# Kernel tuning notes

Measured on AMD Instinct MI355X. Metric: run time of the kernel, lower is better.

The kernel has to match this reference:

```python
import jax, jax.numpy as jnp
import numpy as np

B, L, D, T = 2, 2048, 1536, 2
INITRANGE = 0.1

def setup_inputs() -> dict:
    key = jax.random.key(0)
    k1, k2 = jax.random.split(key)
    hidden_states = jax.random.normal(k1, (B, L, D), dtype=jnp.float32)
    # decoder: Linear(2*D, T) with uniform(-0.1, 0.1) weight, zero bias
    W = jax.random.uniform(k2, (T, 2 * D), dtype=jnp.float32, minval=-INITRANGE, maxval=INITRANGE)
    b = jnp.zeros((T,), dtype=jnp.float32)
    return {"hidden_states": hidden_states, "W": W, "b": b}

def reference(hidden_states, W, b):
    # Faithful fused version of:
    #   prod = h[:,:,None,:] * h[:,None,:,:]; diff = h[:,:,None,:] - h[:,None,:,:]
    #   logits = cat(prod, diff, -1) @ W.T + b
    # Split W into the product half and the difference half.
    d = hidden_states.shape[-1]
    Wp, Wd = W[:, :d], W[:, d:]                      # [T, D] each
    # prod term: sum_d h[b,i,d] * h[b,j,d] * Wp[t,d]
    hw = jnp.einsum('bid,td->btid', hidden_states, Wp)          # [B,T,L,D]
    prod_logits = jnp.einsum('btid,bjd->bijt', hw, hidden_states)  # [B,L,L,T]
    # diff term: (h[b,i]-h[b,j]) @ Wd.T = (h@Wd.T)[b,i] - (h@Wd.T)[b,j]
    hd = jnp.einsum('bid,td->bit', hidden_states, Wd)           # [B,L,T]
    diff_logits = hd[:, :, None, :] - hd[:, None, :, :]         # [B,L,L,T]
    logits = prod_logits + diff_logits + b
    # symmetrize over the (i, j) pair axes
    logits = (logits + jnp.transpose(logits, (0, 2, 1, 3))) * 0.5
    return logits
```

## Files before the change

kernel.cpp:

```cpp
#include <hip/hip_runtime.h>
#include <hip/hip_bf16.h>
#include <stdint.h>

#define B_ 2
#define L_ 2048
#define D_ 1536
#define NT (D_ / 64)

typedef __attribute__((ext_vector_type(4))) float  f32x4;
typedef __attribute__((ext_vector_type(8))) __bf16 bf16x8;

__device__ __forceinline__ unsigned short f2bf(float f) {
  unsigned int u = __float_as_uint(f);
  u += 0x7fffu + ((u >> 16) & 1u);
  return (unsigned short)(u >> 16);
}

__global__ __launch_bounds__(256) void conv_kernel(
    const float* __restrict__ hs, const float* __restrict__ W,
    unsigned short* __restrict__ X, unsigned short* __restrict__ P) {
  const int idx  = blockIdx.x * 256 + threadIdx.x;
  const int base = idx * 4;
  const int d    = base % D_;
  const float4 h  = *(const float4*)(hs + base);
  const float4 w0 = *(const float4*)(W + d);
  const float4 w1 = *(const float4*)(W + 2 * D_ + d);
  ushort4 x, p0, p1;
  x.x  = f2bf(h.x);        x.y  = f2bf(h.y);        x.z  = f2bf(h.z);        x.w  = f2bf(h.w);
  p0.x = f2bf(h.x * w0.x); p0.y = f2bf(h.y * w0.y); p0.z = f2bf(h.z * w0.z); p0.w = f2bf(h.w * w0.w);
  p1.x = f2bf(h.x * w1.x); p1.y = f2bf(h.y * w1.y); p1.z = f2bf(h.z * w1.z); p1.w = f2bf(h.w * w1.w);
  *(ushort4*)(X + base) = x;
  *(ushort4*)(P + base) = p0;
  *(ushort4*)(P + (size_t)B_ * L_ * D_ + base) = p1;
}

__device__ __forceinline__ void gload16(const unsigned short* g, unsigned short* l) {
  __builtin_amdgcn_global_load_lds(
      (const __attribute__((address_space(1))) unsigned int*)g,
      (__attribute__((address_space(3))) unsigned int*)l, 16, 0, 0);
}

#define A0OFF 0
#define A1OFF 8192
#define B0OFF 16384
#define B1OFF 24576

__global__ __launch_bounds__(512, 2) void gemm_kernel(
    const unsigned short* __restrict__ X, const unsigned short* __restrict__ P,
    const float* __restrict__ bias, float2* __restrict__ out) {
  __shared__ unsigned short lds[65536];

  const int tid = threadIdx.x;

  const int id  = blockIdx.x;
  const int swz = (id & 7) * 32 + (id >> 3);
  const int bz  = swz >> 7;
  const int t2  = swz & 127;
  const int I0  = (t2 >> 3) * 128;
  const int J0  = (t2 & 7) * 256;

  const size_t planeB = (size_t)B_ * L_ * D_;
  const unsigned short* gA0 = P + (size_t)(bz * L_ + I0) * D_;
  const unsigned short* gA1 = gA0 + planeB;
  const unsigned short* gB0 = X + (size_t)(bz * L_ + J0) * D_;
  const unsigned short* gB1 = gB0 + (size_t)128 * D_;

  const int    sr    = tid >> 3;
  const int    sc    = (tid & 7) ^ (sr & 7);
  const size_t lgoff = (size_t)sr * D_ + (size_t)(sc * 8);
  const int    wuni  = (tid >> 6) * 512;

  const int lane = tid & 63;
  const int w    = tid >> 6;
  const int wr   = w & 1;
  const int wc   = w >> 1;
  const int lr   = lane & 15;
  const int q    = lane >> 4;
  const int swd  = lr & 7;
  const int csw0 = ((0 + q) ^ swd) * 8;
  const int csw1 = ((4 + q) ^ swd) * 8;
  int aRow[4], bRow[2];
#pragma unroll
  for (int m = 0; m < 4; ++m) aRow[m] = (wr * 64 + m * 16 + lr) * 64;
#pragma unroll
  for (int n = 0; n < 2; ++n) bRow[n] = (wc * 32 + n * 16 + lr) * 64;

  f32x4  acc[8][4] = {};
  bf16x8 aF[4][2], bF[2][2];

#define STG(REG, GBASE, KTN)                                                  \
  do {                                                                        \
    const unsigned short* g0 = (GBASE) + lgoff + (size_t)((KTN) * 64);        \
    gload16(g0,                 lds + (REG) + wuni);                          \
    gload16(g0 + (size_t)64 * D_, lds + (REG) + 4096 + wuni);                 \
  } while (0)

#define RDA(CB, MH)                                                           \
  do {                                                                        \
    _Pragma("unroll") for (int m = 0; m < 4; ++m) {                           \
      aF[m][0] = *(const bf16x8*)(lds + (CB) + (MH) * 8192 + aRow[m] + csw0); \
      aF[m][1] = *(const bf16x8*)(lds + (CB) + (MH) * 8192 + aRow[m] + csw1); \
    }                                                                         \
  } while (0)

#define RDB(CB, NH)                                                           \
  do {                                                                        \
    _Pragma("unroll") for (int n = 0; n < 2; ++n) {                           \
      bF[n][0] = *(const bf16x8*)(lds + (CB) + 16384 + (NH) * 8192 + bRow[n] + csw0); \
      bF[n][1] = *(const bf16x8*)(lds + (CB) + 16384 + (NH) * 8192 + bRow[n] + csw1); \
    }                                                                         \
  } while (0)

#define MM(MH, NH)                                                            \
  do {                                                                        \
    _Pragma("unroll") for (int kk = 0; kk < 2; ++kk)                          \
    _Pragma("unroll") for (int m = 0; m < 4; ++m)                             \
    _Pragma("unroll") for (int n = 0; n < 2; ++n)                             \
      acc[(MH) * 4 + m][(NH) * 2 + n] = __builtin_amdgcn_mfma_f32_16x16x32_bf16( \
          aF[m][kk], bF[n][kk], acc[(MH) * 4 + m][(NH) * 2 + n], 0, 0, 0);    \
  } while (0)

#define BAR()   __builtin_amdgcn_s_barrier()
#define LGKM0() asm volatile("s_waitcnt lgkmcnt(0)" ::: "memory")
#define WVM(n)  asm volatile("s_waitcnt vmcnt(" #n ")" ::: "memory")
#define PRIO1() __builtin_amdgcn_s_setprio(1)
#define PRIO0() __builtin_amdgcn_s_setprio(0)

#define KSTEP(CB, NB, KTN)                                                    \
  do {                                                                        \
                                                                      \
    RDA(CB, 0); RDB(CB, 0);                                                   \
    STG((NB) + A0OFF, gA0, KTN); STG((NB) + B0OFF, gB0, KTN);                 \
    BAR(); LGKM0();                                                           \
    PRIO1(); MM(0, 0); PRIO0();                                               \
    WVM(6); BAR();                                                            \
                                                                      \
    RDB(CB, 1);                                                               \
    STG((NB) + B1OFF, gB1, KTN);                                              \
    BAR(); LGKM0();                                                           \
    PRIO1(); MM(0, 1); PRIO0();                                               \
    WVM(6); BAR();                                                            \
                                                                      \
    RDA(CB, 1);                                                               \
    STG((NB) + A1OFF, gA1, KTN);                                              \
    BAR(); LGKM0();                                                           \
    PRIO1(); MM(1, 1); PRIO0();                                               \
    BAR();                                                                    \
                                        \
    RDB(CB, 0);                                                               \
    BAR(); LGKM0();                                                           \
    PRIO1(); MM(1, 0); PRIO0();                                               \
    WVM(4); BAR();                                                            \
  } while (0)

#define KTAIL(CB)                                                             \
  do {                                                                        \
    RDA(CB, 0); RDB(CB, 0);                                                   \
    BAR(); LGKM0();                                                           \
    PRIO1(); MM(0, 0); PRIO0();                                               \
    WVM(2); BAR();                                                            \
    RDB(CB, 1);                                                               \
    BAR(); LGKM0();                                                           \
    PRIO1(); MM(0, 1); PRIO0();                                               \
    WVM(0); BAR();                                                            \
    RDA(CB, 1);                                                               \
    BAR(); LGKM0();                                                           \
    PRIO1(); MM(1, 1); PRIO0();                                               \
    BAR();                                                                    \
    RDB(CB, 0);                                                               \
    LGKM0();                                                                  \
    PRIO1(); MM(1, 0); PRIO0();                                               \
  } while (0)

  STG(A0OFF, gA0, 0); STG(B0OFF, gB0, 0);
  STG(B1OFF, gB1, 0);
  STG(A1OFF, gA1, 0);
  WVM(4); BAR();

#pragma unroll 1
  for (int it = 0; it < 11; ++it) {
    const int kt0 = 2 * it;
    KSTEP(0,     32768, kt0 + 1);
    KSTEP(32768, 0,     kt0 + 2);
  }
  KSTEP(0, 32768, 23);
  KTAIL(32768);

#undef KSTEP
#undef KTAIL
#undef STG
#undef RDA
#undef RDB
#undef MM

  const float bias0 = bias[0], bias1 = bias[1];
#pragma unroll
  for (int m = 0; m < 4; ++m) {
#pragma unroll
    for (int r = 0; r < 4; ++r) {
      const int i = I0 + wr * 64 + m * 16 + q * 4 + r;
      float2* orow = out + (size_t)(bz * L_ + i) * L_;
#pragma unroll
      for (int n = 0; n < 4; ++n) {
        const int j = J0 + (n >> 1) * 128 + wc * 32 + (n & 1) * 16 + lr;
        float2 v;
        v.x = acc[m][n][r] + bias0;
        v.y = acc[m + 4][n][r] + bias1;
        orow[j] = v;
      }
    }
  }
}

extern "C" void kernel_launch(void* const* d_in, const int* in_sizes, int n_in,
                              void* d_out, int out_size, void* d_ws, size_t ws_size,
                              hipStream_t stream) {
  const float* hs   = (const float*)d_in[0];
  const float* W    = (const float*)d_in[1];
  const float* bias = (const float*)d_in[2];

  unsigned short* X = (unsigned short*)d_ws;
  unsigned short* P = X + (size_t)B_ * L_ * D_;

  const int nconv = (B_ * L_ * D_ / 4) / 256;
  conv_kernel<<<nconv, 256, 0, stream>>>(hs, W, X, P);

  gemm_kernel<<<256, 512, 0, stream>>>(X, P, bias, (float2*)d_out);
}
```

Baseline: 134.6 us.

## Split K-tile into two 32-wide halves with full-tile MFMA phases

Reorganizes the LDS layout so each 64-wide K tile is stored as two 32-column halves with a 4-slot XOR swizzle. Each half is loaded with one 4-operand staging step and consumed by a single phase that reads all A and B fragments and issues all 32 MFMAs. This replaces four sub-phases per K step with two, halving barriers and waitcnt points and enlarging MFMA bursts. The cost is more fragment registers live at once (8 A and 4 B vectors) and a different bank-conflict pattern from the new swizzle.

```diff
diff --git a/kernel.cpp b/kernel.cpp
--- a/kernel.cpp
+++ b/kernel.cpp
@@ -5,7 +5,6 @@
 #define B_ 2
 #define L_ 2048
 #define D_ 1536
-#define NT (D_ / 64)
 
 typedef __attribute__((ext_vector_type(4))) float  f32x4;
 typedef __attribute__((ext_vector_type(8))) __bf16 bf16x8;
@@ -40,11 +39,6 @@
       (__attribute__((address_space(3))) unsigned int*)l, 16, 0, 0);
 }
 
-#define A0OFF 0
-#define A1OFF 8192
-#define B0OFF 16384
-#define B1OFF 24576
-
 __global__ __launch_bounds__(512, 2) void gemm_kernel(
     const unsigned short* __restrict__ X, const unsigned short* __restrict__ P,
     const float* __restrict__ bias, float2* __restrict__ out) {
@@ -60,15 +54,14 @@
   const int J0  = (t2 & 7) * 256;
 
   const size_t planeB = (size_t)B_ * L_ * D_;
-  const unsigned short* gA0 = P + (size_t)(bz * L_ + I0) * D_;
-  const unsigned short* gA1 = gA0 + planeB;
-  const unsigned short* gB0 = X + (size_t)(bz * L_ + J0) * D_;
-  const unsigned short* gB1 = gB0 + (size_t)128 * D_;
 
-  const int    sr    = tid >> 3;
-  const int    sc    = (tid & 7) ^ (sr & 7);
-  const size_t lgoff = (size_t)sr * D_ + (size_t)(sc * 8);
-  const int    wuni  = (tid >> 6) * 512;
+  const size_t gsrcOff = (size_t)(tid >> 2) * D_ +
+                         (size_t)((((tid & 3) ^ ((tid >> 3) & 3))) * 8);
+  const unsigned short* sA0 = P + (size_t)(bz * L_ + I0) * D_ + gsrcOff;
+  const unsigned short* sA1 = sA0 + planeB;
+  const unsigned short* sB0 = X + (size_t)(bz * L_ + J0) * D_ + gsrcOff;
+  const unsigned short* sB1 = sB0 + (size_t)128 * D_;
+  const int wuni = (tid >> 6) * 512;
 
   const int lane = tid & 63;
   const int w    = tid >> 6;
@@ -76,48 +69,42 @@
   const int wc   = w >> 1;
   const int lr   = lane & 15;
   const int q    = lane >> 4;
-  const int swd  = lr & 7;
-  const int csw0 = ((0 + q) ^ swd) * 8;
-  const int csw1 = ((4 + q) ^ swd) * 8;
-  int aRow[4], bRow[2];
+  const int slot8 = ((q ^ ((lr >> 1) & 3)) * 8);
+  int aOff[8], bOff[4];
 #pragma unroll
-  for (int m = 0; m < 4; ++m) aRow[m] = (wr * 64 + m * 16 + lr) * 64;
+  for (int m = 0; m < 8; ++m)
+    aOff[m] = (m >> 2) * 4096 + (wr * 64 + (m & 3) * 16 + lr) * 32;
 #pragma unroll
-  for (int n = 0; n < 2; ++n) bRow[n] = (wc * 32 + n * 16 + lr) * 64;
+  for (int n = 0; n < 4; ++n)
+    bOff[n] = 8192 + (n >> 1) * 4096 + (wc * 32 + (n & 1) * 16 + lr) * 32;
 
   f32x4  acc[8][4] = {};
-  bf16x8 aF[4][2], bF[2][2];
+  bf16x8 aF[8], bF[4];
 
-#define STG(REG, GBASE, KTN)                                                  \
+#define STG4(NB, KH, KTN)                                                     \
   do {                                                                        \
-    const unsigned short* g0 = (GBASE) + lgoff + (size_t)((KTN) * 64);        \
-    gload16(g0,                 lds + (REG) + wuni);                          \
-    gload16(g0 + (size_t)64 * D_, lds + (REG) + 4096 + wuni);                 \
+    const size_t ko = (size_t)((KTN) * 64 + (KH) * 32);                       \
+    gload16(sA0 + ko, lds + (NB) + (KH) * 16384 + 0     + wuni);              \
+    gload16(sA1 + ko, lds + (NB) + (KH) * 16384 + 4096  + wuni);              \
+    gload16(sB0 + ko, lds + (NB) + (KH) * 16384 + 8192  + wuni);              \
+    gload16(sB1 + ko, lds + (NB) + (KH) * 16384 + 12288 + wuni);              \
   } while (0)
 
-#define RDA(CB, MH)                                                           \
+#define RDALL(CB, KH)                                                         \
   do {                                                                        \
-    _Pragma("unroll") for (int m = 0; m < 4; ++m) {                           \
-      aF[m][0] = *(const bf16x8*)(lds + (CB) + (MH) * 8192 + aRow[m] + csw0); \
-      aF[m][1] = *(const bf16x8*)(lds + (CB) + (MH) * 8192 + aRow[m] + csw1); \
-    }                                                                         \
+    const unsigned short* base_ = lds + (CB) + (KH) * 16384 + slot8;          \
+    _Pragma("unroll") for (int m = 0; m < 8; ++m)                             \
+      aF[m] = *(const bf16x8*)(base_ + aOff[m]);                              \
+    _Pragma("unroll") for (int n = 0; n < 4; ++n)                             \
+      bF[n] = *(const bf16x8*)(base_ + bOff[n]);                              \
   } while (0)
 
-#define RDB(CB, NH)                                                           \
+#define MMALL()                                                               \
   do {                                                                        \
-    _Pragma("unroll") for (int n = 0; n < 2; ++n) {                           \
-      bF[n][0] = *(const bf16x8*)(lds + (CB) + 16384 + (NH) * 8192 + bRow[n] + csw0); \
-      bF[n][1] = *(const bf16x8*)(lds + (CB) + 16384 + (NH) * 8192 + bRow[n] + csw1); \
-    }                                                                         \
-  } while (0)
-
-#define MM(MH, NH)                                                            \
-  do {                                                                        \
-    _Pragma("unroll") for (int kk = 0; kk < 2; ++kk)                          \
-    _Pragma("unroll") for (int m = 0; m < 4; ++m)                             \
-    _Pragma("unroll") for (int n = 0; n < 2; ++n)                             \
-      acc[(MH) * 4 + m][(NH) * 2 + n] = __builtin_amdgcn_mfma_f32_16x16x32_bf16( \
-          aF[m][kk], bF[n][kk], acc[(MH) * 4 + m][(NH) * 2 + n], 0, 0, 0);    \
+    _Pragma("unroll") for (int m = 0; m < 8; ++m)                             \
+      _Pragma("unroll") for (int n = 0; n < 4; ++n)                           \
+        acc[m][n] = __builtin_amdgcn_mfma_f32_16x16x32_bf16(                  \
+            aF[m], bF[n], acc[m][n], 0, 0, 0);                                \
   } while (0)
 
 #define BAR()   __builtin_amdgcn_s_barrier()
@@ -128,53 +115,31 @@
 
 #define KSTEP(CB, NB, KTN)                                                    \
   do {                                                                        \
-                                                                      \
-    RDA(CB, 0); RDB(CB, 0);                                                   \
-    STG((NB) + A0OFF, gA0, KTN); STG((NB) + B0OFF, gB0, KTN);                 \
+                                                                \
+    RDALL(CB, 0); STG4(NB, 0, KTN);                                           \
     BAR(); LGKM0();                                                           \
-    PRIO1(); MM(0, 0); PRIO0();                                               \
-    WVM(6); BAR();                                                            \
-                                                                      \
-    RDB(CB, 1);                                                               \
-    STG((NB) + B1OFF, gB1, KTN);                                              \
+    PRIO1(); MMALL(); PRIO0();                                                \
+    WVM(4); BAR();                                                            \
+                                                                \
+    RDALL(CB, 1); STG4(NB, 1, KTN);                                           \
     BAR(); LGKM0();                                                           \
-    PRIO1(); MM(0, 1); PRIO0();                                               \
-    WVM(6); BAR();                                                            \
-                                                                      \
-    RDA(CB, 1);                                                               \
-    STG((NB) + A1OFF, gA1, KTN);                                              \
-    BAR(); LGKM0();                                                           \
-    PRIO1(); MM(1, 1); PRIO0();                                               \
-    BAR();                                                                    \
-                                        \
-    RDB(CB, 0);                                                               \
-    BAR(); LGKM0();                                                           \
-    PRIO1(); MM(1, 0); PRIO0();                                               \
+    PRIO1(); MMALL(); PRIO0();                                                \
     WVM(4); BAR();                                                            \
   } while (0)
 
 #define KTAIL(CB)                                                             \
   do {                                                                        \
-    RDA(CB, 0); RDB(CB, 0);                                                   \
+    RDALL(CB, 0);                                                             \
     BAR(); LGKM0();                                                           \
-    PRIO1(); MM(0, 0); PRIO0();                                               \
-    WVM(2); BAR();                                                            \
-    RDB(CB, 1);                                                               \
-    BAR(); LGKM0();                                                           \
-    PRIO1(); MM(0, 1); PRIO0();                                               \
+    PRIO1(); MMALL(); PRIO0();                                                \
     WVM(0); BAR();                                                            \
-    RDA(CB, 1);                                                               \
-    BAR(); LGKM0();                                                           \
-    PRIO1(); MM(1, 1); PRIO0();                                               \
-    BAR();                                                                    \
-    RDB(CB, 0);                                                               \
+    RDALL(CB, 1);                                                             \
     LGKM0();                                                                  \
-    PRIO1(); MM(1, 0); PRIO0();                                               \
+    PRIO1(); MMALL(); PRIO0();                                                \
   } while (0)
 
-  STG(A0OFF, gA0, 0); STG(B0OFF, gB0, 0);
-  STG(B1OFF, gB1, 0);
-  STG(A1OFF, gA1, 0);
+  STG4(0, 0, 0);
+  STG4(0, 1, 0);
   WVM(4); BAR();
 
 #pragma unroll 1
@@ -188,10 +153,9 @@
 
 #undef KSTEP
 #undef KTAIL
-#undef STG
-#undef RDA
-#undef RDB
-#undef MM
+#undef STG4
+#undef RDALL
+#undef MMALL
 
   const float bias0 = bias[0], bias1 = bias[1];
 #pragma unroll
```

Result: slower. 139.9 us (+3.9%).
